# Kernel optimization log

Measured on AMD Instinct MI355X. Metric: run time of the kernel, lower is better.

Reference implementation:

```python
import jax, jax.numpy as jnp
import numpy as np

EPS = 1e-5

def conv1x1(h, w, b):
    # h: [B,C,H,W], w: [O,C], b: [O]
    return jnp.einsum('bchw,oc->bohw', h, w) + b[None, :, None, None]

def setup_inputs() -> dict:
    key = jax.random.key(0)
    ks = jax.random.split(key, 10)
    B, C, H, W = 4, 256, 64, 64
    x = jax.random.normal(ks[0], (B, C, H, W), dtype=jnp.float32)
    s = 0.02
    return {
        'x': x,
        'gamma': jnp.ones((C,), jnp.float32),
        'beta': jnp.zeros((C,), jnp.float32),
        'wq': jax.random.normal(ks[1], (C, C), jnp.float32) * s,
        'bq': jnp.zeros((C,), jnp.float32),
        'wk': jax.random.normal(ks[2], (C, C), jnp.float32) * s,
        'bk': jnp.zeros((C,), jnp.float32),
        'wv': jax.random.normal(ks[3], (C, C), jnp.float32) * s,
        'bv': jnp.zeros((C,), jnp.float32),
        'wp': jax.random.normal(ks[4], (C, C), jnp.float32) * s,
        'bp': jnp.zeros((C,), jnp.float32),
    }

def reference(x, gamma, beta, wq, bq, wk, bk, wv, bv, wp, bp):
    B, C, H, W = x.shape
    N = H * W
    # BatchNorm2d (training mode: batch statistics, biased variance)
    mean = jnp.mean(x, axis=(0, 2, 3))
    var = jnp.var(x, axis=(0, 2, 3))
    h = (x - mean[None, :, None, None]) * jax.lax.rsqrt(var + EPS)[None, :, None, None]
    h = h * gamma[None, :, None, None] + beta[None, :, None, None]
    q = conv1x1(h, wq, bq).reshape(B, C, N)
    k = conv1x1(h, wk, bk).reshape(B, C, N)
    v = conv1x1(h, wv, bv).reshape(B, C, N)
    # scores[b,i,j] = q_i . k_j, softmax over j (keys)
    scores = jnp.einsum('bci,bcj->bij', q, k) * (C ** -0.5)
    attn = jax.nn.softmax(scores, axis=2)
    # out[b,c,i] = sum_j attn[b,i,j] * v[b,c,j]
    out = jnp.einsum('bij,bcj->bci', attn, v).reshape(B, C, H, W)
    out = conv1x1(out, wp, bp)
    return x + out
```

## Files before the change

### kernel.cpp

```cpp
#include <hip/hip_runtime.h>
#include <cstdint>
#include <cstddef>

#define B_ 4
#define C_ 256
#define N_ 4096

typedef __attribute__((ext_vector_type(8))) short s8v;
typedef __attribute__((ext_vector_type(4))) float f4v;
typedef __attribute__((ext_vector_type(16))) float f16v;
typedef long long i64f;

#if defined(__has_builtin)
#if __has_builtin(__builtin_amdgcn_exp2f)
#define EXP2(x) __builtin_amdgcn_exp2f(x)
#endif
#endif
#ifndef EXP2
#define EXP2(x) exp2f(x)
#endif

#define SCHED_FENCE() __builtin_amdgcn_sched_barrier(0)

__device__ __forceinline__ unsigned short f2bf(float f) {
  unsigned int u = __builtin_bit_cast(unsigned int, f);
  return (unsigned short)((u + 0x7FFFu + ((u >> 16) & 1u)) >> 16);
}

__device__ __forceinline__ float bf2f(unsigned short u) {
  return __builtin_bit_cast(float, (unsigned)u << 16);
}

__device__ __forceinline__ f16v zf16() {
  f16v z;
#pragma unroll
  for (int i = 0; i < 16; ++i) z[i] = 0.f;
  return z;
}


__global__ __launch_bounds__(256) void bn_stats(const float* __restrict__ x,
                                                float* __restrict__ mean,
                                                float* __restrict__ rstd) {
  int c = blockIdx.x, t = threadIdx.x;
  float s = 0.f, s2 = 0.f;
  for (int b = 0; b < B_; ++b) {
    const float* p = x + ((size_t)b * C_ + c) * N_;
    for (int n = t; n < N_; n += 256) { float v = p[n]; s += v; s2 += v * v; }
  }
  __shared__ float rs[256], rs2[256];
  rs[t] = s; rs2[t] = s2; __syncthreads();
  for (int off = 128; off > 0; off >>= 1) {
    if (t < off) { rs[t] += rs[t + off]; rs2[t] += rs2[t + off]; }
    __syncthreads();
  }
  if (t == 0) {
    float m = rs[0] * (1.f / 16384.f);
    float v = rs2[0] * (1.f / 16384.f) - m * m;
    mean[c] = m; rstd[c] = rsqrtf(v + 1e-5f);
  }
}

__global__ __launch_bounds__(256) void prep(
    const float* __restrict__ wq, const float* __restrict__ bq,
    const float* __restrict__ wk, const float* __restrict__ bk,
    const float* __restrict__ wv, const float* __restrict__ bv,
    const float* __restrict__ wp,
    const float* __restrict__ gamma, const float* __restrict__ beta,
    const float* __restrict__ mean, const float* __restrict__ rstd,
    unsigned short* __restrict__ wqb, unsigned short* __restrict__ wkb,
    unsigned short* __restrict__ wvb, unsigned short* __restrict__ wpb,
    float* __restrict__ beq, float* __restrict__ bek, float* __restrict__ bev) {
  const float QSC = 0.0625f * 1.4426950408889634f;
  int o = blockIdx.x, c = threadIdx.x;
  float a = gamma[c] * rstd[c];
  float d = beta[c] - mean[c] * a;
  float wqv = wq[o * C_ + c], wkv = wk[o * C_ + c], wvv = wv[o * C_ + c];
  wqb[o * C_ + c] = f2bf(wqv * a * QSC);
  wkb[o * C_ + c] = f2bf(wkv * a);
  wvb[o * C_ + c] = f2bf(wvv * a);
  wpb[o * C_ + c] = f2bf(wp[o * C_ + c]);
  __shared__ float r0[256], r1[256], r2[256];
  r0[c] = wqv * d; r1[c] = wkv * d; r2[c] = wvv * d; __syncthreads();
  for (int off = 128; off > 0; off >>= 1) {
    if (c < off) { r0[c] += r0[c + off]; r1[c] += r1[c + off]; r2[c] += r2[c + off]; }
    __syncthreads();
  }
  if (c == 0) {
    beq[o] = (bq[o] + r0[0]) * QSC;
    bek[o] = bk[o] + r1[0];
    bev[o] = bv[o] + r2[0];
  }
}

__global__ __launch_bounds__(256) void qkv(
    const float* __restrict__ x,
    const unsigned short* __restrict__ wqb, const unsigned short* __restrict__ wkb,
    const unsigned short* __restrict__ wvb,
    const float* __restrict__ beq, const float* __restrict__ bek,
    const float* __restrict__ bev,
    unsigned short* __restrict__ qB, unsigned short* __restrict__ kB,
    unsigned char* __restrict__ vB) {
  int b = blockIdx.z, oblk = blockIdx.y, n0 = blockIdx.x * 64;
  int tid = threadIdx.x, w = tid >> 6, l = tid & 63, quad = l >> 4, lq = l & 15;
  int orow = oblk * 64 + w * 16 + lq;

  __shared__ unsigned short XF[16384];
  __shared__ unsigned short Ls[64][72];

  {
    int cw = tid >> 6, nl = tid & 63;
    for (int cq = 0; cq < 4; ++cq) {
#pragma unroll
      for (int rr = 0; rr < 16; ++rr) {
        int c = cq * 64 + cw * 16 + rr;
        Ls[nl][cw * 16 + rr] = f2bf(x[((size_t)b * C_ + c) * N_ + n0 + nl]);
      }
      __syncthreads();
      int n_ = tid >> 2, cs = (tid & 3) * 16;
      s8v v0 = *(const s8v*)(&Ls[n_][cs]);
      s8v v1 = *(const s8v*)(&Ls[n_][cs + 8]);
      int fr = ((n_ >> 4) * 32 + ((cq * 64 + cs) >> 3)) * 128 + (n_ & 15) * 8;
      *(s8v*)(XF + fr) = v0;
      *(s8v*)(XF + fr + 128) = v1;
      __syncthreads();
    }
  }

  f4v aq[4], ak[4], av[4];
#pragma unroll
  for (int nt = 0; nt < 4; ++nt) {
    aq[nt] = (f4v){0.f, 0.f, 0.f, 0.f};
    ak[nt] = (f4v){0.f, 0.f, 0.f, 0.f};
    av[nt] = (f4v){0.f, 0.f, 0.f, 0.f};
  }

#pragma unroll
  for (int kk = 0; kk < 8; ++kk) {
    s8v afq = *(const s8v*)(wqb + (size_t)orow * C_ + kk * 32 + quad * 8);
    s8v afk = *(const s8v*)(wkb + (size_t)orow * C_ + kk * 32 + quad * 8);
    s8v afv = *(const s8v*)(wvb + (size_t)orow * C_ + kk * 32 + quad * 8);
#pragma unroll
    for (int nt = 0; nt < 4; ++nt) {
      s8v bf = *(const s8v*)(XF + (nt * 32 + kk * 4 + quad) * 128 + lq * 8);
      aq[nt] = __builtin_amdgcn_mfma_f32_16x16x32_bf16(afq, bf, aq[nt], 0, 0, 0);
      ak[nt] = __builtin_amdgcn_mfma_f32_16x16x32_bf16(afk, bf, ak[nt], 0, 0, 0);
      av[nt] = __builtin_amdgcn_mfma_f32_16x16x32_bf16(afv, bf, av[nt], 0, 0, 0);
    }
  }

  int obase = oblk * 64;

  for (int pass = 0; pass < 2; ++pass) {
    const f4v* acc = (pass == 0) ? aq : ak;
    const float* BE = (pass == 0) ? beq : bek;
    int ob4 = obase + w * 16 + quad * 4;
    float b0 = BE[ob4], b1 = BE[ob4 + 1], b2 = BE[ob4 + 2], b3 = BE[ob4 + 3];
    __syncthreads();
#pragma unroll
    for (int nt = 0; nt < 4; ++nt) {
      unsigned lo = (unsigned)f2bf(acc[nt][0] + b0) | ((unsigned)f2bf(acc[nt][1] + b1) << 16);
      unsigned hi = (unsigned)f2bf(acc[nt][2] + b2) | ((unsigned)f2bf(acc[nt][3] + b3) << 16);
      uint2 pr; pr.x = lo; pr.y = hi;
      *(uint2*)(&Ls[nt * 16 + lq][w * 16 + quad * 4]) = pr;
    }
    __syncthreads();
    {
      unsigned short* dp = (pass == 0) ? qB : kB;
#pragma unroll
      for (int ii = 0; ii < 2; ++ii) {
        int i = tid + ii * 256;
        int g = i >> 8, cs = (i >> 6) & 3, ll = i & 63;
        s8v vv = *(const s8v*)(&Ls[g * 32 + (ll & 31)][cs * 16 + ((ll >> 5) << 3)]);
        size_t dst;
        if (pass == 0)
          dst = ((((size_t)b * 64 + (n0 >> 6)) * 2 + g) * 16 + (obase >> 4) + cs) * 512 + (size_t)ll * 8;
        else
          dst = (((size_t)b * 128 + (n0 >> 5) + g) * 16 + (obase >> 4) + cs) * 512 + (size_t)ll * 8;
        *(s8v*)(dp + dst) = vv;
      }
    }
  }
  __syncthreads();

#pragma unroll
  for (int nt = 0; nt < 4; ++nt)
#pragma unroll
    for (int r = 0; r < 4; ++r) {
      int o_ = obase + w * 16 + quad * 4 + r;
      Ls[w * 16 + quad * 4 + r][nt * 16 + lq] = f2bf(av[nt][r] + bev[o_]);
    }
  __syncthreads();
  {
#pragma unroll
    for (int ii = 0; ii < 2; ++ii) {
      int i = tid + ii * 256;
      int g = i >> 8, ks = (i >> 6) & 3, ll = i & 63;
      s8v vv = *(const s8v*)(&Ls[g * 32 + (ll & 31)][ks * 16 + ((ll >> 5) << 3)]);
      unsigned w0 = (unsigned)__builtin_amdgcn_cvt_pk_fp8_f32(
          bf2f((unsigned short)vv[0]), bf2f((unsigned short)vv[1]), 0, false);
      w0 = (unsigned)__builtin_amdgcn_cvt_pk_fp8_f32(
          bf2f((unsigned short)vv[2]), bf2f((unsigned short)vv[3]), (int)w0, true);
      unsigned w1 = (unsigned)__builtin_amdgcn_cvt_pk_fp8_f32(
          bf2f((unsigned short)vv[4]), bf2f((unsigned short)vv[5]), 0, false);
      w1 = (unsigned)__builtin_amdgcn_cvt_pk_fp8_f32(
          bf2f((unsigned short)vv[6]), bf2f((unsigned short)vv[7]), (int)w1, true);
      uint2 pr; pr.x = w0; pr.y = w1;
      size_t dst = ((((size_t)b * 8 + (obase >> 5) + g) * 256 + (n0 >> 4) + ks) * 64 + ll) * 8;
      *(uint2*)(vB + dst) = pr;
    }
  }
}

__global__ __launch_bounds__(512, 2) void attn(
    const unsigned short* __restrict__ qB, const unsigned short* __restrict__ kB,
    const unsigned char* __restrict__ vB,
    const unsigned short* __restrict__ wpb, const float* __restrict__ bp,
    const float* __restrict__ x, float* __restrict__ out) {
  int id = blockIdx.x;
  int b = (id & 7) >> 1;
  int i0 = (((id >> 3) << 1) | (id & 1)) << 6;
  int tid = threadIdx.x, w = tid >> 6, l = tid & 63;
  int lh = l >> 5, l31 = l & 31;

  __shared__ unsigned short Qs[16384];
  __shared__ unsigned char Ps[2][16384];
  __shared__ unsigned short aS[16384];
  __shared__ float Lw[8][2][32];

  {
    const s8v* g = (const s8v*)(qB + ((size_t)b * 64 + (i0 >> 6)) * 16384);
    s8v* sq = (s8v*)Qs;
    sq[tid] = g[tid];
    sq[tid + 512] = g[tid + 512];
    sq[tid + 1024] = g[tid + 1024];
    sq[tid + 1536] = g[tid + 1536];
  }

  const unsigned short* kp = kB + (((size_t)b * 128 + w) * 16) * 512 + (size_t)l * 8;
  const unsigned char* vp = vB + (((size_t)b * 8 + w) * 256) * 512 + (size_t)l * 8;
  const unsigned short* Qp = Qs + (size_t)lh * 256 + l31 * 8;

  s8v kf[16];
#pragma unroll
  for (int cs = 0; cs < 16; ++cs) kf[cs] = *(const s8v*)(kp + cs * 512);
  SCHED_FENCE();

  __syncthreads();

  f16v O0 = zf16(), O1 = zf16();
  float ls0 = 0.f, ls1 = 0.f;

  for (int t = 0; t < 16; ++t) {
    i64f vf[16];
#pragma unroll
    for (int ks = 0; ks < 16; ++ks) vf[ks] = *(const i64f*)(vp + ks * 512);
    SCHED_FENCE();
    f16v S0 = zf16(), S1 = zf16();
    __builtin_amdgcn_s_setprio(1);
#pragma unroll
    for (int cs = 0; cs < 16; ++cs) {
      s8v q0 = *(const s8v*)(Qp + cs * 512);
      s8v q1 = *(const s8v*)(Qp + 8192 + cs * 512);
      S0 = __builtin_amdgcn_mfma_f32_32x32x16_bf16(kf[cs], q0, S0, 0, 0, 0);
      S1 = __builtin_amdgcn_mfma_f32_32x32x16_bf16(kf[cs], q1, S1, 0, 0, 0);
    }
    __builtin_amdgcn_s_setprio(0);
    SCHED_FENCE();
    unsigned char* Pw = Ps[t & 1] + (w * 4) * 512 + l31 * 8 + lh * 4;
#pragma unroll
    for (int j = 0; j < 4; ++j) {
      float a0 = EXP2(S0[4 * j + 0]), a1 = EXP2(S0[4 * j + 1]);
      float a2 = EXP2(S0[4 * j + 2]), a3 = EXP2(S0[4 * j + 3]);
      ls0 += (a0 + a1) + (a2 + a3);
      unsigned p0 = (unsigned)__builtin_amdgcn_cvt_pk_fp8_f32(a0, a1, 0, false);
      p0 = (unsigned)__builtin_amdgcn_cvt_pk_fp8_f32(a2, a3, (int)p0, true);
      *(unsigned*)(Pw + j * 512) = p0;
      float c0 = EXP2(S1[4 * j + 0]), c1 = EXP2(S1[4 * j + 1]);
      float c2 = EXP2(S1[4 * j + 2]), c3 = EXP2(S1[4 * j + 3]);
      ls1 += (c0 + c1) + (c2 + c3);
      unsigned p1 = (unsigned)__builtin_amdgcn_cvt_pk_fp8_f32(c0, c1, 0, false);
      p1 = (unsigned)__builtin_amdgcn_cvt_pk_fp8_f32(c2, c3, (int)p1, true);
      *(unsigned*)(Pw + j * 512 + 256) = p1;
    }
    __syncthreads();
    kp += 65536;
#pragma unroll
    for (int cs = 0; cs < 16; ++cs) kf[cs] = *(const s8v*)(kp + cs * 512);
    SCHED_FENCE();
    const unsigned char* Pr = Ps[t & 1] + (size_t)lh * 512 + l31 * 8;
    __builtin_amdgcn_s_setprio(1);
#pragma unroll
    for (int ks = 0; ks < 16; ++ks) {
      i64f p0 = *(const i64f*)(Pr + ks * 1024);
      i64f p1 = *(const i64f*)(Pr + ks * 1024 + 256);
      O0 = __builtin_amdgcn_mfma_f32_32x32x16_fp8_fp8(vf[ks], p0, O0, 0, 0, 0);
      O1 = __builtin_amdgcn_mfma_f32_32x32x16_fp8_fp8(vf[ks], p1, O1, 0, 0, 0);
    }
    __builtin_amdgcn_s_setprio(0);
    vp += 8192;
  }

  s8v wf[16];
#pragma unroll
  for (int cs = 0; cs < 16; ++cs)
    wf[cs] = *(const s8v*)(wpb + (size_t)(w * 32 + l31) * 256 + cs * 16 + lh * 8);
  SCHED_FENCE();

  ls0 += __shfl_xor(ls0, 32);
  ls1 += __shfl_xor(ls1, 32);
  if (l < 32) { Lw[w][0][l] = ls0; Lw[w][1][l] = ls1; }
  __syncthreads();
  float s0 = 0.f, s1 = 0.f;
#pragma unroll
  for (int ww = 0; ww < 8; ++ww) { s0 += Lw[ww][0][l31]; s1 += Lw[ww][1][l31]; }
  float rl0 = 1.f / s0, rl1 = 1.f / s1;

#pragma unroll
  for (int jj = 0; jj < 4; ++jj) {
    ushort4 pk;
    pk.x = f2bf(O0[4 * jj + 0] * rl0); pk.y = f2bf(O0[4 * jj + 1] * rl0);
    pk.z = f2bf(O0[4 * jj + 2] * rl0); pk.w = f2bf(O0[4 * jj + 3] * rl0);
    int f0 = ((l31 >> 4) * 32 + w * 4 + jj) * 128 + (l31 & 15) * 8 + lh * 4;
    *(ushort4*)(aS + f0) = pk;
    pk.x = f2bf(O1[4 * jj + 0] * rl1); pk.y = f2bf(O1[4 * jj + 1] * rl1);
    pk.z = f2bf(O1[4 * jj + 2] * rl1); pk.w = f2bf(O1[4 * jj + 3] * rl1);
    int f1 = ((2 + (l31 >> 4)) * 32 + w * 4 + jj) * 128 + (l31 & 15) * 8 + lh * 4;
    *(ushort4*)(aS + f1) = pk;
  }
  __syncthreads();

  f16v OP0 = zf16(), OP1 = zf16();
#pragma unroll
  for (int cs = 0; cs < 16; ++cs) {
    s8v pa0 = *(const s8v*)(aS + ((0 + (l31 >> 4)) * 32 + cs * 2 + lh) * 128 + (l31 & 15) * 8);
    s8v pa1 = *(const s8v*)(aS + ((2 + (l31 >> 4)) * 32 + cs * 2 + lh) * 128 + (l31 & 15) * 8);
    OP0 = __builtin_amdgcn_mfma_f32_32x32x16_bf16(wf[cs], pa0, OP0, 0, 0, 0);
    OP1 = __builtin_amdgcn_mfma_f32_32x32x16_bf16(wf[cs], pa1, OP1, 0, 0, 0);
  }

#pragma unroll
  for (int r = 0; r < 16; ++r) {
    int o_ = w * 32 + (r & 3) + 8 * (r >> 2) + 4 * lh;
    float bpv = bp[o_];
    size_t ix = ((size_t)b * C_ + o_) * N_ + i0 + l31;
    out[ix]      = x[ix]      + OP0[r] + bpv;
    out[ix + 32] = x[ix + 32] + OP1[r] + bpv;
  }
}

extern "C" void kernel_launch(void* const* d_in, const int* in_sizes, int n_in,
                              void* d_out, int out_size, void* d_ws, size_t ws_size,
                              hipStream_t stream) {
  const float* x     = (const float*)d_in[0];
  const float* gamma = (const float*)d_in[1];
  const float* beta  = (const float*)d_in[2];
  const float* wq    = (const float*)d_in[3];
  const float* bq    = (const float*)d_in[4];
  const float* wk    = (const float*)d_in[5];
  const float* bk    = (const float*)d_in[6];
  const float* wv    = (const float*)d_in[7];
  const float* bv    = (const float*)d_in[8];
  const float* wp    = (const float*)d_in[9];
  const float* bp    = (const float*)d_in[10];
  float* out = (float*)d_out;

  char* ws = (char*)d_ws;
  float* mean = (float*)ws; ws += 1024;
  float* rstd = (float*)ws; ws += 1024;
  float* beq  = (float*)ws; ws += 1024;
  float* bek  = (float*)ws; ws += 1024;
  float* bev  = (float*)ws; ws += 1024;
  unsigned short* wqb = (unsigned short*)ws; ws += C_ * C_ * 2;
  unsigned short* wkb = (unsigned short*)ws; ws += C_ * C_ * 2;
  unsigned short* wvb = (unsigned short*)ws; ws += C_ * C_ * 2;
  unsigned short* wpb = (unsigned short*)ws; ws += C_ * C_ * 2;
  unsigned short* qB  = (unsigned short*)ws; ws += (size_t)B_ * N_ * C_ * 2;
  unsigned short* kB  = (unsigned short*)ws; ws += (size_t)B_ * N_ * C_ * 2;
  unsigned char*  vB  = (unsigned char*)ws;  ws += (size_t)B_ * N_ * C_ * 2;

  hipLaunchKernelGGL(bn_stats, dim3(C_), dim3(256), 0, stream, x, mean, rstd);
  hipLaunchKernelGGL(prep, dim3(C_), dim3(256), 0, stream,
                     wq, bq, wk, bk, wv, bv, wp, gamma, beta, mean, rstd,
                     wqb, wkb, wvb, wpb, beq, bek, bev);
  hipLaunchKernelGGL(qkv, dim3(N_ / 64, 4, B_), dim3(256), 0, stream,
                     x, wqb, wkb, wvb, beq, bek, bev, qB, kB, vB);
  hipLaunchKernelGGL(attn, dim3(256), dim3(512), 0, stream,
                     qB, kB, vB, wpb, bp, x, out);
}
```

Baseline: 199.6 us.

## Halve attention query tile to 32 rows and double grid for occupancy

The attention kernel now handles 32 query rows per block instead of 64, launching 512 blocks and raising launch bounds to 4 blocks per CU. Shared memory shrinks: Q and P buffers halve and the output staging reuses the Q buffer. The Q layout written by the qkv kernel is unified with the K layout to match. The V fragment load moves after the QK MFMA loop, presumably to shorten register live ranges. Each K/V tile is now reused by only one query tile instead of two, so K and V global traffic doubles in exchange for more parallelism and latency hiding.

```diff
diff --git a/kernel.cpp b/kernel.cpp
--- a/kernel.cpp
+++ b/kernel.cpp
@@ -172,11 +172,7 @@
         int i = tid + ii * 256;
         int g = i >> 8, cs = (i >> 6) & 3, ll = i & 63;
         s8v vv = *(const s8v*)(&Ls[g * 32 + (ll & 31)][cs * 16 + ((ll >> 5) << 3)]);
-        size_t dst;
-        if (pass == 0)
-          dst = ((((size_t)b * 64 + (n0 >> 6)) * 2 + g) * 16 + (obase >> 4) + cs) * 512 + (size_t)ll * 8;
-        else
-          dst = (((size_t)b * 128 + (n0 >> 5) + g) * 16 + (obase >> 4) + cs) * 512 + (size_t)ll * 8;
+        size_t dst = (((size_t)b * 128 + (n0 >> 5) + g) * 16 + (obase >> 4) + cs) * 512 + (size_t)ll * 8;
         *(s8v*)(dp + dst) = vv;
       }
     }
@@ -212,34 +208,32 @@
   }
 }
 
-__global__ __launch_bounds__(512, 2) void attn(
+__global__ __launch_bounds__(512, 4) void attn(
     const unsigned short* __restrict__ qB, const unsigned short* __restrict__ kB,
     const unsigned char* __restrict__ vB,
     const unsigned short* __restrict__ wpb, const float* __restrict__ bp,
     const float* __restrict__ x, float* __restrict__ out) {
   int id = blockIdx.x;
   int b = (id & 7) >> 1;
-  int i0 = (((id >> 3) << 1) | (id & 1)) << 6;
+  int r32 = ((id >> 3) << 1) | (id & 1);
+  int i0 = r32 << 5;
   int tid = threadIdx.x, w = tid >> 6, l = tid & 63;
   int lh = l >> 5, l31 = l & 31;
 
-  __shared__ unsigned short Qs[16384];
-  __shared__ unsigned char Ps[2][16384];
-  __shared__ unsigned short aS[16384];
-  __shared__ float Lw[8][2][32];
+  __shared__ unsigned short Qs[8192];
+  __shared__ unsigned char Ps[2][8192];
+  __shared__ float Lw[8][32];
 
   {
-    const s8v* g = (const s8v*)(qB + ((size_t)b * 64 + (i0 >> 6)) * 16384);
+    const s8v* g = (const s8v*)(qB + (((size_t)b * 128 + r32) * 16) * 512);
     s8v* sq = (s8v*)Qs;
     sq[tid] = g[tid];
     sq[tid + 512] = g[tid + 512];
-    sq[tid + 1024] = g[tid + 1024];
-    sq[tid + 1536] = g[tid + 1536];
   }
 
   const unsigned short* kp = kB + (((size_t)b * 128 + w) * 16) * 512 + (size_t)l * 8;
   const unsigned char* vp = vB + (((size_t)b * 8 + w) * 256) * 512 + (size_t)l * 8;
-  const unsigned short* Qp = Qs + (size_t)lh * 256 + l31 * 8;
+  const unsigned short* Qp = Qs + (size_t)l * 8;
 
   s8v kf[16];
 #pragma unroll
@@ -248,26 +242,25 @@
 
   __syncthreads();
 
-  f16v O0 = zf16(), O1 = zf16();
-  float ls0 = 0.f, ls1 = 0.f;
+  f16v O0 = zf16();
+  float ls0 = 0.f;
 
   for (int t = 0; t < 16; ++t) {
-    i64f vf[16];
-#pragma unroll
-    for (int ks = 0; ks < 16; ++ks) vf[ks] = *(const i64f*)(vp + ks * 512);
-    SCHED_FENCE();
-    f16v S0 = zf16(), S1 = zf16();
+    f16v S0 = zf16();
     __builtin_amdgcn_s_setprio(1);
 #pragma unroll
     for (int cs = 0; cs < 16; ++cs) {
       s8v q0 = *(const s8v*)(Qp + cs * 512);
-      s8v q1 = *(const s8v*)(Qp + 8192 + cs * 512);
       S0 = __builtin_amdgcn_mfma_f32_32x32x16_bf16(kf[cs], q0, S0, 0, 0, 0);
-      S1 = __builtin_amdgcn_mfma_f32_32x32x16_bf16(kf[cs], q1, S1, 0, 0, 0);
     }
     __builtin_amdgcn_s_setprio(0);
     SCHED_FENCE();
-    unsigned char* Pw = Ps[t & 1] + (w * 4) * 512 + l31 * 8 + lh * 4;
+    i64f vf[16];
+#pragma unroll
+    for (int ks = 0; ks < 16; ++ks) vf[ks] = *(const i64f*)(vp + ks * 512);
+    vp += 8192;
+    SCHED_FENCE();
+    unsigned char* Pw = Ps[t & 1] + w * 1024 + l31 * 8 + lh * 4;
 #pragma unroll
     for (int j = 0; j < 4; ++j) {
       float a0 = EXP2(S0[4 * j + 0]), a1 = EXP2(S0[4 * j + 1]);
@@ -275,30 +268,21 @@
       ls0 += (a0 + a1) + (a2 + a3);
       unsigned p0 = (unsigned)__builtin_amdgcn_cvt_pk_fp8_f32(a0, a1, 0, false);
       p0 = (unsigned)__builtin_amdgcn_cvt_pk_fp8_f32(a2, a3, (int)p0, true);
-      *(unsigned*)(Pw + j * 512) = p0;
-      float c0 = EXP2(S1[4 * j + 0]), c1 = EXP2(S1[4 * j + 1]);
-      float c2 = EXP2(S1[4 * j + 2]), c3 = EXP2(S1[4 * j + 3]);
-      ls1 += (c0 + c1) + (c2 + c3);
-      unsigned p1 = (unsigned)__builtin_amdgcn_cvt_pk_fp8_f32(c0, c1, 0, false);
-      p1 = (unsigned)__builtin_amdgcn_cvt_pk_fp8_f32(c2, c3, (int)p1, true);
-      *(unsigned*)(Pw + j * 512 + 256) = p1;
+      *(unsigned*)(Pw + j * 256) = p0;
     }
     __syncthreads();
     kp += 65536;
 #pragma unroll
     for (int cs = 0; cs < 16; ++cs) kf[cs] = *(const s8v*)(kp + cs * 512);
     SCHED_FENCE();
-    const unsigned char* Pr = Ps[t & 1] + (size_t)lh * 512 + l31 * 8;
+    const unsigned char* Pr = Ps[t & 1] + (size_t)lh * 256 + l31 * 8;
     __builtin_amdgcn_s_setprio(1);
 #pragma unroll
     for (int ks = 0; ks < 16; ++ks) {
-      i64f p0 = *(const i64f*)(Pr + ks * 1024);
-      i64f p1 = *(const i64f*)(Pr + ks * 1024 + 256);
+      i64f p0 = *(const i64f*)(Pr + ks * 512);
       O0 = __builtin_amdgcn_mfma_f32_32x32x16_fp8_fp8(vf[ks], p0, O0, 0, 0, 0);
-      O1 = __builtin_amdgcn_mfma_f32_32x32x16_fp8_fp8(vf[ks], p1, O1, 0, 0, 0);
     }
     __builtin_amdgcn_s_setprio(0);
-    vp += 8192;
   }
 
   s8v wf[16];
@@ -308,14 +292,14 @@
   SCHED_FENCE();
 
   ls0 += __shfl_xor(ls0, 32);
-  ls1 += __shfl_xor(ls1, 32);
-  if (l < 32) { Lw[w][0][l] = ls0; Lw[w][1][l] = ls1; }
-  __syncthreads();
-  float s0 = 0.f, s1 = 0.f;
-#pragma unroll
-  for (int ww = 0; ww < 8; ++ww) { s0 += Lw[ww][0][l31]; s1 += Lw[ww][1][l31]; }
-  float rl0 = 1.f / s0, rl1 = 1.f / s1;
-
+  if (l < 32) Lw[w][l] = ls0;
+  __syncthreads();
+  float s0 = 0.f;
+#pragma unroll
+  for (int ww = 0; ww < 8; ++ww) s0 += Lw[ww][l31];
+  float rl0 = 1.f / s0;
+
+  unsigned short* aS = Qs;
 #pragma unroll
   for (int jj = 0; jj < 4; ++jj) {
     ushort4 pk;
@@ -323,29 +307,21 @@
     pk.z = f2bf(O0[4 * jj + 2] * rl0); pk.w = f2bf(O0[4 * jj + 3] * rl0);
     int f0 = ((l31 >> 4) * 32 + w * 4 + jj) * 128 + (l31 & 15) * 8 + lh * 4;
     *(ushort4*)(aS + f0) = pk;
-    pk.x = f2bf(O1[4 * jj + 0] * rl1); pk.y = f2bf(O1[4 * jj + 1] * rl1);
-    pk.z = f2bf(O1[4 * jj + 2] * rl1); pk.w = f2bf(O1[4 * jj + 3] * rl1);
-    int f1 = ((2 + (l31 >> 4)) * 32 + w * 4 + jj) * 128 + (l31 & 15) * 8 + lh * 4;
-    *(ushort4*)(aS + f1) = pk;
-  }
-  __syncthreads();
-
-  f16v OP0 = zf16(), OP1 = zf16();
+  }
+  __syncthreads();
+
+  f16v OP0 = zf16();
 #pragma unroll
   for (int cs = 0; cs < 16; ++cs) {
-    s8v pa0 = *(const s8v*)(aS + ((0 + (l31 >> 4)) * 32 + cs * 2 + lh) * 128 + (l31 & 15) * 8);
-    s8v pa1 = *(const s8v*)(aS + ((2 + (l31 >> 4)) * 32 + cs * 2 + lh) * 128 + (l31 & 15) * 8);
+    s8v pa0 = *(const s8v*)(aS + ((l31 >> 4) * 32 + cs * 2 + lh) * 128 + (l31 & 15) * 8);
     OP0 = __builtin_amdgcn_mfma_f32_32x32x16_bf16(wf[cs], pa0, OP0, 0, 0, 0);
-    OP1 = __builtin_amdgcn_mfma_f32_32x32x16_bf16(wf[cs], pa1, OP1, 0, 0, 0);
   }
 
 #pragma unroll
   for (int r = 0; r < 16; ++r) {
     int o_ = w * 32 + (r & 3) + 8 * (r >> 2) + 4 * lh;
-    float bpv = bp[o_];
     size_t ix = ((size_t)b * C_ + o_) * N_ + i0 + l31;
-    out[ix]      = x[ix]      + OP0[r] + bpv;
-    out[ix + 32] = x[ix + 32] + OP1[r] + bpv;
+    out[ix] = x[ix] + OP0[r] + bp[o_];
   }
 }
 
@@ -385,6 +361,6 @@
                      wqb, wkb, wvb, wpb, beq, bek, bev);
   hipLaunchKernelGGL(qkv, dim3(N_ / 64, 4, B_), dim3(256), 0, stream,
                      x, wqb, wkb, wvb, beq, bek, bev, qB, kB, vB);
-  hipLaunchKernelGGL(attn, dim3(256), dim3(512), 0, stream,
+  hipLaunchKernelGGL(attn, dim3(512), dim3(512), 0, stream,
                      qB, kB, vB, wpb, bp, x, out);
 }
```

Result: slower. 387.3 us (+94.1%).
